# Kernel tuning notes

Hardware: AMD Instinct MI355X
Metric: run time of the kernel (lower is better)

The kernel has to match this reference:

```python
import jax, jax.numpy as jnp
import numpy as np

N, E = 10000, 160000
DIN, H, DOUT, DE = 128, 256, 256, 32


def _lin(k, din, dout, scale=0.05):
    return jax.random.normal(k, (din, dout), jnp.float32) * scale


def setup_inputs() -> dict:
    key = jax.random.key(0)
    ks = jax.random.split(key, 40)
    inp = {}
    inp["x"] = jax.random.normal(ks[0], (N, DIN), jnp.float32)
    inp["edge_attr"] = jax.random.normal(ks[1], (E, DE), jnp.float32)
    inp["src"] = jax.random.randint(ks[2], (E,), 0, N, jnp.int32)
    inp["dst"] = jax.random.randint(ks[3], (E,), 0, N, jnp.int32)
    # encoders
    inp["W_edge_enc"] = _lin(ks[4], DE, H); inp["b_edge_enc"] = jnp.zeros((H,), jnp.float32)
    inp["W_node_enc"] = _lin(ks[5], DIN, H); inp["b_node_enc"] = jnp.zeros((H,), jnp.float32)
    # 3 TransformerConv layers (heads=1): q,k,v (with bias), edge (no bias), skip (with bias)
    outs = [H, H, DOUT]
    i = 6
    for l, C in enumerate(outs, start=1):
        inp[f"Wq{l}"] = _lin(ks[i], H, C); i += 1
        inp[f"bq{l}"] = jnp.zeros((C,), jnp.float32)
        inp[f"Wk{l}"] = _lin(ks[i], H, C); i += 1
        inp[f"bk{l}"] = jnp.zeros((C,), jnp.float32)
        inp[f"Wv{l}"] = _lin(ks[i], H, C); i += 1
        inp[f"bv{l}"] = jnp.zeros((C,), jnp.float32)
        inp[f"We{l}"] = _lin(ks[i], H, C); i += 1
        inp[f"Ws{l}"] = _lin(ks[i], H, C); i += 1
        inp[f"bs{l}"] = jnp.zeros((C,), jnp.float32)
    return inp


def _tconv(x, src, dst, edge_emb, Wq, bq, Wk, bk, Wv, bv, We, Ws, bs):
    # PyG TransformerConv, heads=1, concat=True, root_weight=True
    n = x.shape[0]
    C = Wq.shape[1]
    q = x @ Wq + bq            # [N, C]
    k = x @ Wk + bk            # [N, C]
    v = x @ Wv + bv            # [N, C]
    e = edge_emb @ We          # [E, C] (lin_edge, no bias)
    kj = k[src] + e            # [E, C]
    alpha = jnp.sum(q[dst] * kj, axis=-1) / jnp.sqrt(jnp.float32(C))  # [E]
    # segment softmax over incoming edges per target node
    m = jax.ops.segment_max(alpha, dst, num_segments=n)
    a = jnp.exp(alpha - m[dst])
    denom = jax.ops.segment_sum(a, dst, num_segments=n)
    a = a / jnp.maximum(denom[dst], 1e-16)
    msg = (v[src] + e) * a[:, None]                       # [E, C]
    out = jax.ops.segment_sum(msg, dst, num_segments=n)   # [N, C]
    return out + x @ Ws + bs                               # root skip


def reference(x, edge_attr, src, dst,
              W_edge_enc, b_edge_enc, W_node_enc, b_node_enc,
              Wq1, bq1, Wk1, bk1, Wv1, bv1, We1, Ws1, bs1,
              Wq2, bq2, Wk2, bk2, Wv2, bv2, We2, Ws2, bs2,
              Wq3, bq3, Wk3, bk3, Wv3, bv3, We3, Ws3, bs3):
    relu = jax.nn.relu
    edge_feat = relu(edge_attr @ W_edge_enc + b_edge_enc)  # [E, H]
    h = relu(x @ W_node_enc + b_node_enc)                  # [N, H]
    # dropout(0.3) is identity in eval mode
    h = relu(_tconv(h, src, dst, edge_feat, Wq1, bq1, Wk1, bk1, Wv1, bv1, We1, Ws1, bs1))
    h = relu(_tconv(h, src, dst, edge_feat, Wq2, bq2, Wk2, bk2, Wv2, bv2, We2, Ws2, bs2))
    h = _tconv(h, src, dst, edge_feat, Wq3, bq3, Wk3, bk3, Wv3, bv3, We3, Ws3, bs3)
    return h
```

## Files before the change

### kernel.cpp

```cpp
#include <hip/hip_runtime.h>
#include <cstdint>

typedef unsigned short u16;
typedef __attribute__((ext_vector_type(8))) short short8;
typedef __attribute__((ext_vector_type(8))) __bf16 bf16x8;
typedef __attribute__((ext_vector_type(4))) float f32x4;

#define DEV __device__ __forceinline__

DEV u16 f2bf(float f){
  uint32_t u = __float_as_uint(f);
  u += 0x7fffu + ((u >> 16) & 1u);
  return (u16)(u >> 16);
}
DEV float bf2f(u16 h){ return __uint_as_float(((uint32_t)h) << 16); }
DEV u16 f2h(float f){ return __builtin_bit_cast(u16, (_Float16)f); }
DEV float h2f(u16 h){ return (float)__builtin_bit_cast(_Float16, h); }

DEV f32x4 mfma16(short8 a, short8 b, f32x4 c){
  return __builtin_amdgcn_mfma_f32_16x16x32_bf16(
      __builtin_bit_cast(bf16x8, a), __builtin_bit_cast(bf16x8, b), c, 0, 0, 0);
}

#define NN 10000
#define EE 160000
#define MPN 10112
#define MPE 160128

__global__ void count_k(const int* __restrict__ dst, int* __restrict__ cnt){
  int i = blockIdx.x * 256 + threadIdx.x;
  if(i < EE) atomicAdd(&cnt[dst[i]], 1);
}

__global__ __launch_bounds__(1024) void scan_k(const int* __restrict__ cnt,
                                               int* __restrict__ offs,
                                               int* __restrict__ cursor){
  __shared__ int psum[1024];
  int tid = threadIdx.x;
  int base = tid * 10;
  int loc[10];
  int s = 0;
  #pragma unroll
  for(int j = 0; j < 10; ++j){
    int idx = base + j;
    int v = (idx < NN) ? cnt[idx] : 0;
    loc[j] = s; s += v;
  }
  psum[tid] = s;
  __syncthreads();
  for(int d = 1; d < 1024; d <<= 1){
    int t = (tid >= d) ? psum[tid - d] : 0;
    __syncthreads();
    psum[tid] += t;
    __syncthreads();
  }
  int add = (tid > 0) ? psum[tid - 1] : 0;
  #pragma unroll
  for(int j = 0; j < 10; ++j){
    int idx = base + j;
    if(idx < NN){ int v = loc[j] + add; offs[idx] = v; cursor[idx] = v; }
  }
  if(tid == 0) offs[NN] = EE;
}

__global__ void scatter_k(const int* __restrict__ dst, int* __restrict__ cursor,
                          int* __restrict__ eids){
  int i = blockIdx.x * 256 + threadIdx.x;
  if(i < EE){ int p = atomicAdd(&cursor[dst[i]], 1); eids[p] = i; }
}

__global__ void rank_k(const int* __restrict__ dst, const int* __restrict__ src,
                       const int* __restrict__ offs, const int* __restrict__ eids,
                       int* __restrict__ eidp, int* __restrict__ srcp){
  int e = blockIdx.x * 256 + threadIdx.x;
  if(e >= MPE) return;
  if(e >= EE){ eidp[e] = e; return; }
  int n = dst[e];
  int p0 = offs[n], p1 = offs[n + 1];
  int rk = 0;
  for(int p = p0; p < p1; ++p) rk += (eids[p] < e) ? 1 : 0;
  int slot = p0 + rk;
  eidp[slot] = e;
  srcp[slot] = src[e];
}

struct WPack {
  const float* Wq[3]; const float* Wk[3]; const float* Wv[3];
  const float* Ws[3]; const float* We[3];
  const float* bq[3]; const float* bk[3]; const float* bv[3]; const float* bs[3];
};

#define PG0 5056
#define PG1 (PG0 + 20016)
#define PG2 (PG1 + 3840)
#define PG3 (PG2 + 1536)
#define PG4 (PG3 + 15)
#define PG5 (PG4 + 256)

__global__ __launch_bounds__(256) void prep_all_k(
    const float* __restrict__ x, const float* __restrict__ eattr, WPack P,
    const float* __restrict__ Wne, const float* __restrict__ Wee,
    u16* __restrict__ xbf, u16* __restrict__ eabf,
    u16* __restrict__ Wcat, u16* __restrict__ Wet,
    u16* __restrict__ WqBF, u16* __restrict__ WeBF,
    float* __restrict__ biasc, u16* __restrict__ Wnet, u16* __restrict__ Weet)
{
  int b = blockIdx.x, tid = threadIdx.x;
  if(b < PG0){
    int i = b * 256 + tid;
    xbf[i] = (i < NN * 128) ? f2bf(x[i]) : (u16)0;
  } else if(b < PG1){
    int i = (b - PG0) * 256 + tid;
    eabf[i] = (i < EE * 32) ? f2bf(eattr[i]) : (u16)0;
  } else if(b < PG2){
    int b2 = b - PG1; int l = b2 / 1280, r = b2 % 1280; int k = tid;
    float v;
    if(r < 256)       v = P.Wq[l][k * 256 + r];
    else if(r < 512)  v = P.Ws[l][k * 256 + (r - 256)];
    else if(r < 768){ Wet[((size_t)l * 256 + (r - 512)) * 256 + k] =
                        f2bf(P.We[l][k * 256 + (r - 512)]); return; }
    else if(r < 1024) v = P.Wk[l][k * 256 + (r - 768)];
    else              v = P.Wv[l][k * 256 + (r - 1024)];
    Wcat[((size_t)l * 1280 + r) * 256 + k] = f2bf(v);
  } else if(b < PG3){
    int b3 = b - PG2; int l = b3 >> 9, rr = b3 & 511; int t = tid;
    if(rr < 256) WqBF[((size_t)l * 256 + rr) * 256 + t] = f2bf(P.Wq[l][rr * 256 + t]);
    else         WeBF[((size_t)l * 256 + (rr - 256)) * 256 + t] = f2bf(P.We[l][(rr - 256) * 256 + t]);
  } else if(b < PG4){
    int b4 = b - PG3; int l = b4 / 5, seg = b4 % 5; int t = tid;
    float v;
    if(seg == 0)      v = P.bq[l][t];
    else if(seg == 1) v = P.bs[l][t];
    else if(seg == 2){
      const float* we = P.We[l] + (size_t)t * 256; const float* bq = P.bq[l];
      float s = 0.f;
      for(int c = 0; c < 256; ++c) s += bq[c] * we[c];
      v = s;
    }
    else if(seg == 3) v = P.bk[l][t];
    else              v = P.bv[l][t];
    biasc[(size_t)l * 1280 + seg * 256 + t] = v;
  } else {
    int n = b - PG4;
    if(tid < 128) Wnet[n * 128 + tid] = f2bf(Wne[(size_t)tid * 256 + n]);
    if(tid < 32)  Weet[n * 32 + tid]  = f2bf(Wee[(size_t)tid * 256 + n]);
  }
}

template<int BK, int EPI, int AG>
DEV void gemm_body(short8* smem8,
    const u16* __restrict__ A, const u16* __restrict__ Bt,
    const float* __restrict__ bias, void* Out,
    const u16* __restrict__ accvH, const u16* __restrict__ skipH,
    const int* __restrict__ rowmap, u16* __restrict__ kvout,
    u16* __restrict__ skipOut,
    int bx, int by, int bz,
    int Mreal, int Nld, int K, size_t sA, size_t sB, size_t sOb)
{
  constexpr int CPR = BK / 8;
  constexpr int SW  = (BK == 64) ? 7 : 3;
  u16* Al = (u16*)smem8;
  u16* Bl = Al + 128 * BK;
  A  += (size_t)bz * sA;
  Bt += (size_t)bz * sB;
  Out = (void*)((char*)Out + (size_t)bz * sOb);
  int tid = threadIdx.x, lane = tid & 63;
  int rowBase = bx * 128, colBase = by * 128;
  int wave = tid >> 6, wm = wave >> 1, wn = wave & 1;
  int lr = lane & 15, lk = lane >> 4;
  f32x4 acc[4][4] = {};
  int nkt = K / BK;
  for(int kt = 0; kt < nkt; ++kt){
    __syncthreads();
    for(int ci = tid; ci < 128 * CPR; ci += 256){
      int r = ci / CPR, cb = ci % CPR;
      int ar = AG ? rowmap[rowBase + r] : (rowBase + r);
      int d = (r * CPR + (cb ^ (r & SW))) * 8;
      *(short8*)&Al[d] = *(const short8*)&A [(size_t)ar * K + kt * BK + cb * 8];
      *(short8*)&Bl[d] = *(const short8*)&Bt[(size_t)(colBase + r) * K + kt * BK + cb * 8];
    }
    __syncthreads();
    #pragma unroll
    for(int kk = 0; kk < BK / 32; ++kk){
      short8 af[4], bfr[4];
      #pragma unroll
      for(int m = 0; m < 4; ++m){
        int r = wm * 64 + m * 16 + lr;
        int byt = r * (BK * 2) + kk * 64 + lk * 16; byt ^= (r & SW) << 4;
        af[m] = *(const short8*)((const char*)Al + byt);
      }
      #pragma unroll
      for(int n = 0; n < 4; ++n){
        int r = wn * 64 + n * 16 + lr;
        int byt = r * (BK * 2) + kk * 64 + lk * 16; byt ^= (r & SW) << 4;
        bfr[n] = *(const short8*)((const char*)Bl + byt);
      }
      #pragma unroll
      for(int m = 0; m < 4; ++m)
        #pragma unroll
        for(int n = 0; n < 4; ++n)
          acc[m][n] = mfma16(af[m], bfr[n], acc[m][n]);
    }
  }

  __syncthreads();
  if constexpr(EPI == 4){
    float* fs = (float*)smem8;
    #pragma unroll
    for(int h = 0; h < 2; ++h){
      if(wm == h){
        #pragma unroll
        for(int m = 0; m < 4; ++m)
          #pragma unroll
          for(int n = 0; n < 4; ++n){
            int cc = wn * 64 + n * 16 + lr;
            int c = colBase + cc;
            #pragma unroll
            for(int j = 0; j < 4; ++j){
              int r2 = m * 16 + lk * 4 + j;
              int r = rowBase + h * 64 + r2;
              fs[r2 * 128 + cc] = acc[m][n][j]
                + h2f(accvH[(size_t)r * 256 + c]) + h2f(skipH[(size_t)r * 256 + c]);
            }
          }
      }
      __syncthreads();
      for(int ch = tid; ch < 2048; ch += 256){
        int rr = ch >> 5, cc = (ch & 31) << 2;
        int r = rowBase + h * 64 + rr;
        if(r < Mreal)
          *(float4*)&((float*)Out)[(size_t)r * Nld + colBase + cc] = *(float4*)&fs[rr * 128 + cc];
      }
      __syncthreads();
    }
  } else if constexpr(EPI == 0){
    int sec = by >> 1;
    u16* us = (u16*)smem8;
    #pragma unroll
    for(int m = 0; m < 4; ++m)
      #pragma unroll
      for(int n = 0; n < 4; ++n){
        int cc = wn * 64 + n * 16 + lr;
        #pragma unroll
        for(int j = 0; j < 4; ++j){
          int rr = wm * 64 + m * 16 + lk * 4 + j;
          float v = acc[m][n][j] + bias[colBase + cc];
          us[rr * 128 + cc] = (sec == 1) ? f2h(v) : f2bf(v);
        }
      }
    __syncthreads();
    u16* dstp; int cofs, ldd;
    if(sec == 0){ dstp = (u16*)Out; cofs = colBase; ldd = 512; }
    else if(sec == 1){ dstp = skipOut; cofs = colBase - 256; ldd = 256; }
    else if(sec == 2){ dstp = (u16*)Out; cofs = colBase - 256; ldd = 512; }
    else { dstp = kvout; cofs = colBase - 768; ldd = 512; }
    for(int ch = tid; ch < 2048; ch += 256){
      int rr = ch >> 4, cc = (ch & 15) << 3;
      int r = rowBase + rr;
      if(r < Mreal)
        *(short8*)&dstp[(size_t)r * ldd + cofs + cc] = *(short8*)&us[rr * 128 + cc];
    }
  } else {
    u16* us = (u16*)smem8;
    #pragma unroll
    for(int m = 0; m < 4; ++m)
      #pragma unroll
      for(int n = 0; n < 4; ++n){
        int cc = wn * 64 + n * 16 + lr;
        int c = colBase + cc;
        #pragma unroll
        for(int j = 0; j < 4; ++j){
          int rr = wm * 64 + m * 16 + lk * 4 + j;
          float v = acc[m][n][j];
          if constexpr(EPI == 1){ v += bias[c]; v = fmaxf(v, 0.f); }
          else if constexpr(EPI == 3){
            int r = rowBase + rr;
            v += h2f(accvH[(size_t)r * 256 + c]) + h2f(skipH[(size_t)r * 256 + c]);
            v = fmaxf(v, 0.f);
          }
          us[rr * 128 + cc] = f2bf(v);
        }
      }
    __syncthreads();
    for(int ch = tid; ch < 2048; ch += 256){
      int rr = ch >> 4, cc = (ch & 15) << 3;
      int r = rowBase + rr;
      if(r < Mreal)
        *(short8*)&((u16*)Out)[(size_t)r * Nld + colBase + cc] = *(short8*)&us[rr * 128 + cc];
    }
  }
}

__global__ __launch_bounds__(256) void slab_k(
    const u16* __restrict__ A, const u16* __restrict__ Bt,
    const float* __restrict__ bias, u16* __restrict__ qq,
    u16* __restrict__ kvout, u16* __restrict__ skipOut){
  __shared__ short8 smem[2048];
  gemm_body<64,0,0>(smem, A, Bt, bias, qq, nullptr, nullptr, nullptr, kvout, skipOut,
                    blockIdx.x, blockIdx.y, 0, NN, 512, 256, 0, 0, 0);
}

__global__ __launch_bounds__(256) void out3_k(
    const u16* __restrict__ A, const u16* __restrict__ Bt, u16* __restrict__ Out,
    const u16* __restrict__ accvH, const u16* __restrict__ skipH){
  __shared__ short8 smem[2048];
  gemm_body<64,3,0>(smem, A, Bt, nullptr, Out, accvH, skipH, nullptr, nullptr, nullptr,
                    blockIdx.x, blockIdx.y, 0, NN, 256, 256, 0, 0, 0);
}

__global__ __launch_bounds__(256) void out4_k(
    const u16* __restrict__ A, const u16* __restrict__ Bt, float* __restrict__ Out,
    const u16* __restrict__ accvH, const u16* __restrict__ skipH){
  __shared__ short8 smem[2048];
  gemm_body<64,4,0>(smem, A, Bt, nullptr, Out, accvH, skipH, nullptr, nullptr, nullptr,
                    blockIdx.x, blockIdx.y, 0, NN, 256, 256, 0, 0, 0);
}

__global__ __launch_bounds__(256) void enc_all_k(
    const u16* __restrict__ xbf, const u16* __restrict__ Wnet,
    const float* __restrict__ bne, u16* __restrict__ hbf,
    const u16* __restrict__ eabf, const u16* __restrict__ Weet,
    const float* __restrict__ bee, u16* __restrict__ efp, const int* __restrict__ eidp,
    const u16* __restrict__ WeBF, const u16* __restrict__ WqBF, u16* __restrict__ WcatQ){
  __shared__ short8 smem[2048];
  int b = blockIdx.x;
  if(b < 158){
    gemm_body<64,1,0>(smem, xbf, Wnet, bne, hbf, nullptr, nullptr, nullptr, nullptr, nullptr,
                      b >> 1, b & 1, 0, NN, 256, 128, 0, 0, 0);
  } else if(b < 2660){
    int bb = b - 158;
    gemm_body<32,1,1>(smem, eabf, Weet, bee, efp, nullptr, nullptr, eidp, nullptr, nullptr,
                      bb >> 1, bb & 1, 0, EE, 256, 32, 0, 0, 0);
  } else {
    int bb = b - 2660;
    gemm_body<64,5,0>(smem, WeBF, WqBF, nullptr, WcatQ, nullptr, nullptr, nullptr, nullptr, nullptr,
                      bb & 1, (bb >> 1) & 1, bb >> 2, 256, 256, 256,
                      (size_t)256 * 256, (size_t)256 * 256, (size_t)1280 * 256 * 2);
  }
}

__global__ __launch_bounds__(256) void node_pass_k(
    const u16* __restrict__ qq, const u16* __restrict__ efp,
    const u16* __restrict__ kvbf,
    const int* __restrict__ srcp, const int* __restrict__ offs,
    u16* __restrict__ accvH, u16* __restrict__ aggef)
{
  int wave = threadIdx.x >> 6, lane = threadIdx.x & 63;
  int n = blockIdx.x * 4 + wave;
  if(n >= NN) return;
  int li = lane & 15, eg = lane >> 4;
  const u16* qrow = qq + (size_t)n * 512 + li * 16;
  short8 qh0 = *(const short8*)(qrow),       qh1 = *(const short8*)(qrow + 8);
  short8 eh0 = *(const short8*)(qrow + 256), eh1 = *(const short8*)(qrow + 264);
  float q[16], e[16];
  #pragma unroll
  for(int d = 0; d < 8; ++d){
    q[d] = bf2f((u16)qh0[d]); q[8 + d] = bf2f((u16)qh1[d]);
    e[d] = bf2f((u16)eh0[d]); e[8 + d] = bf2f((u16)eh1[d]);
  }
  float av[16], ag[16];
  #pragma unroll
  for(int d = 0; d < 16; ++d){ av[d] = 0.f; ag[d] = 0.f; }
  float den = 0.f;
  int p0 = offs[n], pe = offs[n + 1];
  int p = p0 + eg;
  for(; p + 4 < pe; p += 8){
    int s1 = srcp[p], s2 = srcp[p + 4];
    const u16* kv1 = kvbf + ((size_t)s1 << 9) + li * 16;
    const u16* kv2 = kvbf + ((size_t)s2 << 9) + li * 16;
    const u16* e1 = efp + (((size_t)p) << 8) + li * 16;
    const u16* e2 = efp + (((size_t)(p + 4)) << 8) + li * 16;
    short8 kA1 = *(const short8*)(kv1),       kB1 = *(const short8*)(kv1 + 8);
    short8 vA1 = *(const short8*)(kv1 + 256), vB1 = *(const short8*)(kv1 + 264);
    short8 fA1 = *(const short8*)(e1),        fB1 = *(const short8*)(e1 + 8);
    short8 kA2 = *(const short8*)(kv2),       kB2 = *(const short8*)(kv2 + 8);
    short8 vA2 = *(const short8*)(kv2 + 256), vB2 = *(const short8*)(kv2 + 264);
    short8 fA2 = *(const short8*)(e2),        fB2 = *(const short8*)(e2 + 8);
    float sc1 = 0.f, sc2 = 0.f;
    #pragma unroll
    for(int d = 0; d < 8; ++d){
      sc1 += q[d]   * bf2f((u16)kA1[d]) + e[d]   * bf2f((u16)fA1[d]);
      sc1 += q[8+d] * bf2f((u16)kB1[d]) + e[8+d] * bf2f((u16)fB1[d]);
      sc2 += q[d]   * bf2f((u16)kA2[d]) + e[d]   * bf2f((u16)fA2[d]);
      sc2 += q[8+d] * bf2f((u16)kB2[d]) + e[8+d] * bf2f((u16)fB2[d]);
    }
    sc1 += __shfl_xor(sc1, 1); sc2 += __shfl_xor(sc2, 1);
    sc1 += __shfl_xor(sc1, 2); sc2 += __shfl_xor(sc2, 2);
    sc1 += __shfl_xor(sc1, 4); sc2 += __shfl_xor(sc2, 4);
    sc1 += __shfl_xor(sc1, 8); sc2 += __shfl_xor(sc2, 8);
    float w1 = __expf(sc1 * 0.0625f);
    float w2 = __expf(sc2 * 0.0625f);
    den += w1 + w2;
    #pragma unroll
    for(int d = 0; d < 8; ++d){
      av[d]   += w1 * bf2f((u16)vA1[d]) + w2 * bf2f((u16)vA2[d]);
      av[8+d] += w1 * bf2f((u16)vB1[d]) + w2 * bf2f((u16)vB2[d]);
      ag[d]   += w1 * bf2f((u16)fA1[d]) + w2 * bf2f((u16)fA2[d]);
      ag[8+d] += w1 * bf2f((u16)fB1[d]) + w2 * bf2f((u16)fB2[d]);
    }
  }
  if(p < pe){
    int s = srcp[p];
    const u16* kvp = kvbf + ((size_t)s << 9) + li * 16;
    const u16* ep = efp + (((size_t)p) << 8) + li * 16;
    short8 kA = *(const short8*)(kvp),       kB = *(const short8*)(kvp + 8);
    short8 vA = *(const short8*)(kvp + 256), vB = *(const short8*)(kvp + 264);
    short8 fA = *(const short8*)(ep),        fB = *(const short8*)(ep + 8);
    float part = 0.f;
    #pragma unroll
    for(int d = 0; d < 8; ++d){
      part += q[d]   * bf2f((u16)kA[d]) + e[d]   * bf2f((u16)fA[d]);
      part += q[8+d] * bf2f((u16)kB[d]) + e[8+d] * bf2f((u16)fB[d]);
    }
    part += __shfl_xor(part, 1);
    part += __shfl_xor(part, 2);
    part += __shfl_xor(part, 4);
    part += __shfl_xor(part, 8);
    float wgt = __expf(part * 0.0625f);
    den += wgt;
    #pragma unroll
    for(int d = 0; d < 8; ++d){
      av[d]   += wgt * bf2f((u16)vA[d]);
      av[8+d] += wgt * bf2f((u16)vB[d]);
      ag[d]   += wgt * bf2f((u16)fA[d]);
      ag[8+d] += wgt * bf2f((u16)fB[d]);
    }
  }
  #pragma unroll
  for(int d = 0; d < 16; ++d){
    av[d] += __shfl_xor(av[d], 16); av[d] += __shfl_xor(av[d], 32);
    ag[d] += __shfl_xor(ag[d], 16); ag[d] += __shfl_xor(ag[d], 32);
  }
  den += __shfl_xor(den, 16); den += __shfl_xor(den, 32);
  float rden = 1.f / fmaxf(den, 1e-16f);
  if(eg == 0){
    u16* ao = accvH + (size_t)n * 256 + li * 16;
    #pragma unroll
    for(int t = 0; t < 2; ++t){
      short8 o;
      #pragma unroll
      for(int d = 0; d < 8; ++d) o[d] = (short)f2h(av[t*8+d] * rden);
      *(short8*)(ao + t * 8) = o;
    }
  } else if(eg == 1){
    u16* go = aggef + (size_t)n * 256 + li * 16;
    #pragma unroll
    for(int t = 0; t < 2; ++t){
      short8 o;
      #pragma unroll
      for(int d = 0; d < 8; ++d) o[d] = (short)f2bf(ag[t*8+d] * rden);
      *(short8*)(go + t * 8) = o;
    }
  }
}

extern "C" void kernel_launch(void* const* d_in, const int* in_sizes, int n_in,
                              void* d_out, int out_size, void* d_ws, size_t ws_size,
                              hipStream_t stream){
  const float* x     = (const float*)d_in[0];
  const float* eattr = (const float*)d_in[1];
  const int*   src   = (const int*)d_in[2];
  const int*   dst   = (const int*)d_in[3];
  const float* Wee   = (const float*)d_in[4];
  const float* bee   = (const float*)d_in[5];
  const float* Wne   = (const float*)d_in[6];
  const float* bne   = (const float*)d_in[7];
  WPack P;
  for(int l = 0; l < 3; ++l){
    const int b = 8 + l * 9;
    P.Wq[l] = (const float*)d_in[b + 0]; P.bq[l] = (const float*)d_in[b + 1];
    P.Wk[l] = (const float*)d_in[b + 2]; P.bk[l] = (const float*)d_in[b + 3];
    P.Wv[l] = (const float*)d_in[b + 4]; P.bv[l] = (const float*)d_in[b + 5];
    P.We[l] = (const float*)d_in[b + 6];
    P.Ws[l] = (const float*)d_in[b + 7]; P.bs[l] = (const float*)d_in[b + 8];
  }

  char* w = (char*)d_ws; size_t off = 0;
  auto alloc = [&](size_t bytes)->char*{
    char* p = w + off; off = (off + bytes + 255) & ~(size_t)255; return p;
  };
  u16*   Wcat  = (u16*)  alloc((size_t)3 * 1280 * 256 * 2);
  u16*   Wet   = (u16*)  alloc((size_t)3 * 256 * 256 * 2);
  u16*   WqBF  = (u16*)  alloc((size_t)3 * 256 * 256 * 2);
  u16*   WeBF  = (u16*)  alloc((size_t)3 * 256 * 256 * 2);
  float* biasc = (float*)alloc((size_t)3 * 1280 * 4);
  u16*   Wnet  = (u16*)  alloc((size_t)256 * 128 * 2);
  u16*   Weet  = (u16*)  alloc((size_t)256 * 32 * 2);
  u16*   xbf   = (u16*)  alloc((size_t)MPN * 128 * 2);
  u16*   eabf  = (u16*)  alloc((size_t)MPE * 32 * 2);
  u16*   hbf   = (u16*)  alloc((size_t)MPN * 256 * 2);
  u16*   qq    = (u16*)  alloc((size_t)MPN * 512 * 2);
  u16*   skipf = (u16*)  alloc((size_t)MPN * 256 * 2);
  u16*   kvbf  = (u16*)  alloc((size_t)MPN * 512 * 2);
  u16*   efp   = (u16*)  alloc((size_t)MPE * 256 * 2);
  int*   cnt   = (int*)  alloc((size_t)NN * 4);
  int*   offs  = (int*)  alloc((size_t)(NN + 1) * 4);
  int*   cursor= (int*)  alloc((size_t)NN * 4);
  int*   eids  = (int*)  alloc((size_t)EE * 4);
  int*   eidp  = (int*)  alloc((size_t)MPE * 4);
  int*   srcp  = (int*)  alloc((size_t)EE * 4);
  u16*   accv  = (u16*)  alloc((size_t)MPN * 256 * 2);
  u16*   aggef = (u16*)  alloc((size_t)MPN * 256 * 2);
  if(off > ws_size) return;

  hipMemsetAsync(cnt, 0, (size_t)NN * 4, stream);
  count_k <<<(EE + 255) / 256, 256, 0, stream>>>(dst, cnt);
  scan_k  <<<1, 1024, 0, stream>>>(cnt, offs, cursor);
  scatter_k<<<(EE + 255) / 256, 256, 0, stream>>>(dst, cursor, eids);
  rank_k  <<<(MPE + 255) / 256, 256, 0, stream>>>(dst, src, offs, eids, eidp, srcp);

  prep_all_k<<<PG5, 256, 0, stream>>>(x, eattr, P, Wne, Wee,
      xbf, eabf, Wcat, Wet, WqBF, WeBF, biasc, Wnet, Weet);

  enc_all_k<<<2672, 256, 0, stream>>>(
      xbf, Wnet, bne, hbf,
      eabf, Weet, bee, efp, eidp,
      WeBF, WqBF, Wcat + (size_t)512 * 256);

  for(int l = 0; l < 3; ++l){
    slab_k<<<dim3(MPN / 128, 10), 256, 0, stream>>>(
        hbf, Wcat + (size_t)l * 1280 * 256, biasc + (size_t)l * 1280, qq, kvbf, skipf);
    node_pass_k<<<NN / 4, 256, 0, stream>>>(qq, efp, kvbf, srcp, offs, accv, aggef);
    if(l < 2)
      out3_k<<<dim3(MPN / 128, 2), 256, 0, stream>>>(
          aggef, Wet + (size_t)l * 256 * 256, hbf, accv, skipf);
    else
      out4_k<<<dim3(MPN / 128, 2), 256, 0, stream>>>(
          aggef, Wet + (size_t)l * 256 * 256, (float*)d_out, accv, skipf);
  }
}
```

Baseline: 338.6 us.

## Store edge features as FP8 and fold edge counting into prep kernel

```diff
diff --git a/kernel.cpp b/kernel.cpp
--- a/kernel.cpp
+++ b/kernel.cpp
@@ -2,9 +2,11 @@
 #include <cstdint>
 
 typedef unsigned short u16;
+typedef unsigned char u8;
 typedef __attribute__((ext_vector_type(8))) short short8;
 typedef __attribute__((ext_vector_type(8))) __bf16 bf16x8;
 typedef __attribute__((ext_vector_type(4))) float f32x4;
+typedef __attribute__((ext_vector_type(2))) float f32x2;
 
 #define DEV __device__ __forceinline__
 
@@ -17,6 +19,21 @@
 DEV u16 f2h(float f){ return __builtin_bit_cast(u16, (_Float16)f); }
 DEV float h2f(u16 h){ return (float)__builtin_bit_cast(_Float16, h); }
 
+DEV u8 f2fp8(float v){
+  return (u8)(__builtin_amdgcn_cvt_pk_fp8_f32(v, v, 0, false) & 0xff);
+}
+DEV void fp8cvt16(int4 w, float* f){
+  f32x2 p;
+  p = __builtin_amdgcn_cvt_pk_f32_fp8(w.x, false); f[0]=p[0];  f[1]=p[1];
+  p = __builtin_amdgcn_cvt_pk_f32_fp8(w.x, true ); f[2]=p[0];  f[3]=p[1];
+  p = __builtin_amdgcn_cvt_pk_f32_fp8(w.y, false); f[4]=p[0];  f[5]=p[1];
+  p = __builtin_amdgcn_cvt_pk_f32_fp8(w.y, true ); f[6]=p[0];  f[7]=p[1];
+  p = __builtin_amdgcn_cvt_pk_f32_fp8(w.z, false); f[8]=p[0];  f[9]=p[1];
+  p = __builtin_amdgcn_cvt_pk_f32_fp8(w.z, true ); f[10]=p[0]; f[11]=p[1];
+  p = __builtin_amdgcn_cvt_pk_f32_fp8(w.w, false); f[12]=p[0]; f[13]=p[1];
+  p = __builtin_amdgcn_cvt_pk_f32_fp8(w.w, true ); f[14]=p[0]; f[15]=p[1];
+}
+
 DEV f32x4 mfma16(short8 a, short8 b, f32x4 c){
   return __builtin_amdgcn_mfma_f32_16x16x32_bf16(
       __builtin_bit_cast(bf16x8, a), __builtin_bit_cast(bf16x8, b), c, 0, 0, 0);
@@ -26,11 +43,6 @@
 #define EE 160000
 #define MPN 10112
 #define MPE 160128
-
-__global__ void count_k(const int* __restrict__ dst, int* __restrict__ cnt){
-  int i = blockIdx.x * 256 + threadIdx.x;
-  if(i < EE) atomicAdd(&cnt[dst[i]], 1);
-}
 
 __global__ __launch_bounds__(1024) void scan_k(const int* __restrict__ cnt,
                                                int* __restrict__ offs,
@@ -96,10 +108,12 @@
 #define PG3 (PG2 + 1536)
 #define PG4 (PG3 + 15)
 #define PG5 (PG4 + 256)
+#define PG6 (PG5 + 625)
 
 __global__ __launch_bounds__(256) void prep_all_k(
     const float* __restrict__ x, const float* __restrict__ eattr, WPack P,
     const float* __restrict__ Wne, const float* __restrict__ Wee,
+    const int* __restrict__ dst, int* __restrict__ cnt,
     u16* __restrict__ xbf, u16* __restrict__ eabf,
     u16* __restrict__ Wcat, u16* __restrict__ Wet,
     u16* __restrict__ WqBF, u16* __restrict__ WeBF,
@@ -140,10 +154,13 @@
     else if(seg == 3) v = P.bk[l][t];
     else              v = P.bv[l][t];
     biasc[(size_t)l * 1280 + seg * 256 + t] = v;
-  } else {
+  } else if(b < PG5){
     int n = b - PG4;
     if(tid < 128) Wnet[n * 128 + tid] = f2bf(Wne[(size_t)tid * 256 + n]);
     if(tid < 32)  Weet[n * 32 + tid]  = f2bf(Wee[(size_t)tid * 256 + n]);
+  } else {
+    int i = (b - PG5) * 256 + tid;
+    if(i < EE) atomicAdd(&cnt[dst[i]], 1);
   }
 }
 
@@ -233,6 +250,27 @@
       }
       __syncthreads();
     }
+  } else if constexpr(EPI == 2){
+    u8* us = (u8*)smem8;
+    #pragma unroll
+    for(int m = 0; m < 4; ++m)
+      #pragma unroll
+      for(int n = 0; n < 4; ++n){
+        int cc = wn * 64 + n * 16 + lr;
+        #pragma unroll
+        for(int j = 0; j < 4; ++j){
+          int rr = wm * 64 + m * 16 + lk * 4 + j;
+          float v = acc[m][n][j] + bias[colBase + cc];
+          us[rr * 128 + cc] = f2fp8(fmaxf(v, 0.f));
+        }
+      }
+    __syncthreads();
+    for(int ch = tid; ch < 1024; ch += 256){
+      int rr = ch >> 3, cc = (ch & 7) << 4;
+      int r = rowBase + rr;
+      if(r < Mreal)
+        *(int4*)&((u8*)Out)[(size_t)r * Nld + colBase + cc] = *(int4*)&us[rr * 128 + cc];
+    }
   } else if constexpr(EPI == 0){
     int sec = by >> 1;
     u16* us = (u16*)smem8;
@@ -320,7 +358,7 @@
     const u16* __restrict__ xbf, const u16* __restrict__ Wnet,
     const float* __restrict__ bne, u16* __restrict__ hbf,
     const u16* __restrict__ eabf, const u16* __restrict__ Weet,
-    const float* __restrict__ bee, u16* __restrict__ efp, const int* __restrict__ eidp,
+    const float* __restrict__ bee, u8* __restrict__ efp8, const int* __restrict__ eidp,
     const u16* __restrict__ WeBF, const u16* __restrict__ WqBF, u16* __restrict__ WcatQ){
   __shared__ short8 smem[2048];
   int b = blockIdx.x;
@@ -329,7 +367,7 @@
                       b >> 1, b & 1, 0, NN, 256, 128, 0, 0, 0);
   } else if(b < 2660){
     int bb = b - 158;
-    gemm_body<32,1,1>(smem, eabf, Weet, bee, efp, nullptr, nullptr, eidp, nullptr, nullptr,
+    gemm_body<32,2,1>(smem, eabf, Weet, bee, efp8, nullptr, nullptr, eidp, nullptr, nullptr,
                       bb >> 1, bb & 1, 0, EE, 256, 32, 0, 0, 0);
   } else {
     int bb = b - 2660;
@@ -340,7 +378,7 @@
 }
 
 __global__ __launch_bounds__(256) void node_pass_k(
-    const u16* __restrict__ qq, const u16* __restrict__ efp,
+    const u16* __restrict__ qq, const u8* __restrict__ efp8,
     const u16* __restrict__ kvbf,
     const int* __restrict__ srcp, const int* __restrict__ offs,
     u16* __restrict__ accvH, u16* __restrict__ aggef)
@@ -368,21 +406,23 @@
     int s1 = srcp[p], s2 = srcp[p + 4];
     const u16* kv1 = kvbf + ((size_t)s1 << 9) + li * 16;
     const u16* kv2 = kvbf + ((size_t)s2 << 9) + li * 16;
-    const u16* e1 = efp + (((size_t)p) << 8) + li * 16;
-    const u16* e2 = efp + (((size_t)(p + 4)) << 8) + li * 16;
+    const u8* e1 = efp8 + (((size_t)p) << 8) + li * 16;
+    const u8* e2 = efp8 + (((size_t)(p + 4)) << 8) + li * 16;
     short8 kA1 = *(const short8*)(kv1),       kB1 = *(const short8*)(kv1 + 8);
     short8 vA1 = *(const short8*)(kv1 + 256), vB1 = *(const short8*)(kv1 + 264);
-    short8 fA1 = *(const short8*)(e1),        fB1 = *(const short8*)(e1 + 8);
     short8 kA2 = *(const short8*)(kv2),       kB2 = *(const short8*)(kv2 + 8);
     short8 vA2 = *(const short8*)(kv2 + 256), vB2 = *(const short8*)(kv2 + 264);
-    short8 fA2 = *(const short8*)(e2),        fB2 = *(const short8*)(e2 + 8);
+    int4 fw1 = *(const int4*)(e1);
+    int4 fw2 = *(const int4*)(e2);
+    float f1[16], f2[16];
+    fp8cvt16(fw1, f1); fp8cvt16(fw2, f2);
     float sc1 = 0.f, sc2 = 0.f;
     #pragma unroll
     for(int d = 0; d < 8; ++d){
-      sc1 += q[d]   * bf2f((u16)kA1[d]) + e[d]   * bf2f((u16)fA1[d]);
-      sc1 += q[8+d] * bf2f((u16)kB1[d]) + e[8+d] * bf2f((u16)fB1[d]);
-      sc2 += q[d]   * bf2f((u16)kA2[d]) + e[d]   * bf2f((u16)fA2[d]);
-      sc2 += q[8+d] * bf2f((u16)kB2[d]) + e[8+d] * bf2f((u16)fB2[d]);
+      sc1 += q[d]   * bf2f((u16)kA1[d]) + e[d]   * f1[d];
+      sc1 += q[8+d] * bf2f((u16)kB1[d]) + e[8+d] * f1[8+d];
+      sc2 += q[d]   * bf2f((u16)kA2[d]) + e[d]   * f2[d];
+      sc2 += q[8+d] * bf2f((u16)kB2[d]) + e[8+d] * f2[8+d];
     }
     sc1 += __shfl_xor(sc1, 1); sc2 += __shfl_xor(sc2, 1);
     sc1 += __shfl_xor(sc1, 2); sc2 += __shfl_xor(sc2, 2);
@@ -395,22 +435,23 @@
     for(int d = 0; d < 8; ++d){
       av[d]   += w1 * bf2f((u16)vA1[d]) + w2 * bf2f((u16)vA2[d]);
       av[8+d] += w1 * bf2f((u16)vB1[d]) + w2 * bf2f((u16)vB2[d]);
-      ag[d]   += w1 * bf2f((u16)fA1[d]) + w2 * bf2f((u16)fA2[d]);
-      ag[8+d] += w1 * bf2f((u16)fB1[d]) + w2 * bf2f((u16)fB2[d]);
+      ag[d]   += w1 * f1[d]   + w2 * f2[d];
+      ag[8+d] += w1 * f1[8+d] + w2 * f2[8+d];
     }
   }
   if(p < pe){
     int s = srcp[p];
     const u16* kvp = kvbf + ((size_t)s << 9) + li * 16;
-    const u16* ep = efp + (((size_t)p) << 8) + li * 16;
+    const u8* ep = efp8 + (((size_t)p) << 8) + li * 16;
     short8 kA = *(const short8*)(kvp),       kB = *(const short8*)(kvp + 8);
     short8 vA = *(const short8*)(kvp + 256), vB = *(const short8*)(kvp + 264);
-    short8 fA = *(const short8*)(ep),        fB = *(const short8*)(ep + 8);
+    int4 fw = *(const int4*)(ep);
+    float f[16]; fp8cvt16(fw, f);
     float part = 0.f;
     #pragma unroll
     for(int d = 0; d < 8; ++d){
-      part += q[d]   * bf2f((u16)kA[d]) + e[d]   * bf2f((u16)fA[d]);
-      part += q[8+d] * bf2f((u16)kB[d]) + e[8+d] * bf2f((u16)fB[d]);
+      part += q[d]   * bf2f((u16)kA[d]) + e[d]   * f[d];
+      part += q[8+d] * bf2f((u16)kB[d]) + e[8+d] * f[8+d];
     }
     part += __shfl_xor(part, 1);
     part += __shfl_xor(part, 2);
@@ -422,8 +463,8 @@
     for(int d = 0; d < 8; ++d){
       av[d]   += wgt * bf2f((u16)vA[d]);
       av[8+d] += wgt * bf2f((u16)vB[d]);
-      ag[d]   += wgt * bf2f((u16)fA[d]);
-      ag[8+d] += wgt * bf2f((u16)fB[d]);
+      ag[d]   += wgt * f[d];
+      ag[8+d] += wgt * f[8+d];
     }
   }
   #pragma unroll
@@ -492,7 +533,7 @@
   u16*   qq    = (u16*)  alloc((size_t)MPN * 512 * 2);
   u16*   skipf = (u16*)  alloc((size_t)MPN * 256 * 2);
   u16*   kvbf  = (u16*)  alloc((size_t)MPN * 512 * 2);
-  u16*   efp   = (u16*)  alloc((size_t)MPE * 256 * 2);
+  u8*    efp8  = (u8*)   alloc((size_t)MPE * 256);
   int*   cnt   = (int*)  alloc((size_t)NN * 4);
   int*   offs  = (int*)  alloc((size_t)(NN + 1) * 4);
   int*   cursor= (int*)  alloc((size_t)NN * 4);
@@ -504,23 +545,21 @@
   if(off > ws_size) return;
 
   hipMemsetAsync(cnt, 0, (size_t)NN * 4, stream);
-  count_k <<<(EE + 255) / 256, 256, 0, stream>>>(dst, cnt);
+  prep_all_k<<<PG6, 256, 0, stream>>>(x, eattr, P, Wne, Wee, dst, cnt,
+      xbf, eabf, Wcat, Wet, WqBF, WeBF, biasc, Wnet, Weet);
   scan_k  <<<1, 1024, 0, stream>>>(cnt, offs, cursor);
   scatter_k<<<(EE + 255) / 256, 256, 0, stream>>>(dst, cursor, eids);
   rank_k  <<<(MPE + 255) / 256, 256, 0, stream>>>(dst, src, offs, eids, eidp, srcp);
 
-  prep_all_k<<<PG5, 256, 0, stream>>>(x, eattr, P, Wne, Wee,
-      xbf, eabf, Wcat, Wet, WqBF, WeBF, biasc, Wnet, Weet);
-
   enc_all_k<<<2672, 256, 0, stream>>>(
       xbf, Wnet, bne, hbf,
-      eabf, Weet, bee, efp, eidp,
+      eabf, Weet, bee, efp8, eidp,
       WeBF, WqBF, Wcat + (size_t)512 * 256);
 
   for(int l = 0; l < 3; ++l){
     slab_k<<<dim3(MPN / 128, 10), 256, 0, stream>>>(
         hbf, Wcat + (size_t)l * 1280 * 256, biasc + (size_t)l * 1280, qq, kvbf, skipf);
-    node_pass_k<<<NN / 4, 256, 0, stream>>>(qq, efp, kvbf, srcp, offs, accv, aggef);
+    node_pass_k<<<NN / 4, 256, 0, stream>>>(qq, efp8, kvbf, srcp, offs, accv, aggef);
     if(l < 2)
       out3_k<<<dim3(MPN / 128, 2), 256, 0, stream>>>(
           aggef, Wet + (size_t)l * 256 * 256, hbf, accv, skipf);
```

After: 318.5 us. -5.9%, faster.
